# Performance work log

Hardware: AMD Instinct MI355X
Metric: run time of the kernel (lower is better)

## Reference

```python
import jax, jax.numpy as jnp
import numpy as np

EMBED = 768
HEADS = 12
HEAD_DIM = EMBED // HEADS
HIDDEN = int(EMBED * 4.0)
B, N = 2, 2048


def setup_inputs() -> dict:
    key = jax.random.key(0)
    ks = jax.random.split(key, 8)
    s = 0.02
    return {
        "x": jax.random.normal(ks[0], (B, N, EMBED), dtype=jnp.float32),
        "ln1_g": jnp.ones((EMBED,), jnp.float32),
        "ln1_b": jnp.zeros((EMBED,), jnp.float32),
        "qkv_w": jax.random.normal(ks[1], (3 * EMBED, EMBED), jnp.float32) * s,
        "qkv_b": jnp.zeros((3 * EMBED,), jnp.float32),
        "proj_w": jax.random.normal(ks[2], (EMBED, EMBED), jnp.float32) * s,
        "proj_b": jnp.zeros((EMBED,), jnp.float32),
        "ln2_g": jnp.ones((EMBED,), jnp.float32),
        "ln2_b": jnp.zeros((EMBED,), jnp.float32),
        "fc1_w": jax.random.normal(ks[3], (HIDDEN, EMBED), jnp.float32) * s,
        "fc1_b": jnp.zeros((HIDDEN,), jnp.float32),
        "fc2_w": jax.random.normal(ks[4], (EMBED, HIDDEN), jnp.float32) * s,
        "fc2_b": jnp.zeros((EMBED,), jnp.float32),
    }


def _layernorm(x, g, b, eps=1e-5):
    mu = jnp.mean(x, axis=-1, keepdims=True)
    var = jnp.var(x, axis=-1, keepdims=True)
    return (x - mu) * jax.lax.rsqrt(var + eps) * g + b


def reference(x, ln1_g, ln1_b, qkv_w, qkv_b, proj_w, proj_b,
              ln2_g, ln2_b, fc1_w, fc1_b, fc2_w, fc2_b):
    Bs, Ns, C = x.shape
    # --- attention (pre-norm) ---
    h = _layernorm(x, ln1_g, ln1_b)
    qkv = h @ qkv_w.T + qkv_b                      # [B,N,3C]
    qkv = qkv.reshape(Bs, Ns, 3, HEADS, HEAD_DIM)
    q, k, v = qkv[:, :, 0], qkv[:, :, 1], qkv[:, :, 2]   # [B,N,H,D]
    scale = HEAD_DIM ** -0.5
    attn = jnp.einsum('bqhd,bkhd->bhqk', q, k) * scale   # [B,H,N,N]
    attn = jax.nn.softmax(attn, axis=-1)
    o = jnp.einsum('bhqk,bkhd->bqhd', attn, v).reshape(Bs, Ns, C)
    x = x + (o @ proj_w.T + proj_b)
    # --- MLP (pre-norm) ---
    h = _layernorm(x, ln2_g, ln2_b)
    h = jax.nn.gelu(h @ fc1_w.T + fc1_b, approximate=False)  # torch GELU = erf
    x = x + (h @ fc2_w.T + fc2_b)
    return x
```

## Files before the change

### kernel.cpp

```cpp
#include <hip/hip_runtime.h>
#include <stdint.h>

#define EMBED  768
#define HEADS  12
#define HDIM   64
#define HIDDEN 3072
#define BSZ    2
#define SEQ    2048
#define NTOK   4096
#define QKVN   2304

typedef short short8 __attribute__((ext_vector_type(8)));
typedef float f32x4 __attribute__((ext_vector_type(4)));
typedef float float4v __attribute__((ext_vector_type(4)));
typedef unsigned short ushort4v __attribute__((ext_vector_type(4)));

__device__ __forceinline__ unsigned short f2bf(float f) {
    uint32_t x = __builtin_bit_cast(uint32_t, f);
    x = x + 0x7fffu + ((x >> 16) & 1u);
    return (unsigned short)(x >> 16);
}
__device__ __forceinline__ void load16(const void* g, void* l) {
    __builtin_amdgcn_global_load_lds((const __attribute__((address_space(1))) void*)g,
                                     (__attribute__((address_space(3))) void*)l, 16, 0, 0);
}

__global__ __launch_bounds__(256) void cvt4_k(const float* __restrict__ s0, unsigned short* __restrict__ o0, int n0,
                                              const float* __restrict__ s1, unsigned short* __restrict__ o1, int n1,
                                              const float* __restrict__ s2, unsigned short* __restrict__ o2, int n2,
                                              const float* __restrict__ s3, unsigned short* __restrict__ o3, int n3) {
    int i = blockIdx.x * blockDim.x + threadIdx.x;
    const int stride = gridDim.x * blockDim.x;
    const int tot = n0 + n1 + n2 + n3;
    for (; i < tot; i += stride) {
        const float* s; unsigned short* o; int j = i;
        if (j < n0) { s = s0; o = o0; }
        else if ((j -= n0) < n1) { s = s1; o = o1; }
        else if ((j -= n1) < n2) { s = s2; o = o2; }
        else { j -= n2; s = s3; o = o3; }
        float4v v = ((const float4v*)s)[j];
        ushort4v u;
#pragma unroll
        for (int t = 0; t < 4; t++) u[t] = f2bf(v[t]);
        ((ushort4v*)o)[j] = u;
    }
}

__global__ __launch_bounds__(256) void ln_k(const float* __restrict__ x,
                                            const float* __restrict__ g,
                                            const float* __restrict__ b,
                                            unsigned short* __restrict__ out) {
    const int row = blockIdx.x;
    const int t = threadIdx.x;
    const float* xr = x + (size_t)row * EMBED;
    float v0 = xr[t], v1 = xr[t + 256], v2 = xr[t + 512];
    float s = v0 + v1 + v2;
    float s2 = v0 * v0 + v1 * v1 + v2 * v2;
#pragma unroll
    for (int m = 1; m < 64; m <<= 1) { s += __shfl_xor(s, m); s2 += __shfl_xor(s2, m); }
    __shared__ float red[8];
    const int w = t >> 6;
    if ((t & 63) == 0) { red[w] = s; red[4 + w] = s2; }
    __syncthreads();
    s = red[0] + red[1] + red[2] + red[3];
    s2 = red[4] + red[5] + red[6] + red[7];
    const float mu = s * (1.0f / EMBED);
    const float var = s2 * (1.0f / EMBED) - mu * mu;
    const float rs = rsqrtf(var + 1e-5f);
    unsigned short* orow = out + (size_t)row * EMBED;
    orow[t]       = f2bf((v0 - mu) * rs * g[t]       + b[t]);
    orow[t + 256] = f2bf((v1 - mu) * rs * g[t + 256] + b[t + 256]);
    orow[t + 512] = f2bf((v2 - mu) * rs * g[t + 512] + b[t + 512]);
}

template <int EPI>
__global__ __launch_bounds__(256) void gemm_bt(const unsigned short* __restrict__ A,
                                               const unsigned short* __restrict__ W,
                                               const float* __restrict__ bias,
                                               const float* __restrict__ res,
                                               void* __restrict__ outp,
                                               unsigned short* __restrict__ vt,
                                               int M, int N, int K) {
    __shared__ __align__(16) char smem[36864];
    const int tid = threadIdx.x;
    const int w = tid >> 6, l = tid & 63;
    const int lr = l >> 4, lc = l & 15;
    const int nb = N >> 7;

    int bid = blockIdx.x;
    bid = (bid & 7) * (gridDim.x >> 3) + (bid >> 3);
    const int bx = bid % nb, by = bid / nb;
    const int row0 = by << 7, col0 = bx << 7;
    const int wr = w >> 1, wc = w & 1;
    const int srow = tid >> 2, skoff = (tid & 3) * 8;

    f32x4 acc[4][4] = {};

    const unsigned short* Ag0 = A + (size_t)(row0 + srow) * K + skoff;
    const unsigned short* Ag1 = A + (size_t)(row0 + 64 + srow) * K + skoff;
    const unsigned short* Wg0 = W + (size_t)(col0 + srow) * K + skoff;
    const unsigned short* Wg1 = W + (size_t)(col0 + 64 + srow) * K + skoff;

    auto Asb = [&](int buf) -> unsigned short* { return (unsigned short*)(smem + buf * 8192); };
    auto Bsb = [&](int buf) -> unsigned short* { return (unsigned short*)(smem + 16384 + buf * 8192); };

    auto stage = [&](int buf, int k0) {
        load16(Ag0 + k0, Asb(buf) + tid * 8);
        load16(Ag1 + k0, Asb(buf) + 2048 + tid * 8);
        load16(Wg0 + k0, Bsb(buf) + tid * 8);
        load16(Wg1 + k0, Bsb(buf) + 2048 + tid * 8);
    };
    auto compute = [&](int buf) {
        short8 af[4], bfr[4];
#pragma unroll
        for (int i = 0; i < 4; i++) af[i] = *(const short8*)&Asb(buf)[(wr * 64 + i * 16 + lc) * 32 + 8 * lr];
#pragma unroll
        for (int j = 0; j < 4; j++) bfr[j] = *(const short8*)&Bsb(buf)[(wc * 64 + j * 16 + lc) * 32 + 8 * lr];
#pragma unroll
        for (int i = 0; i < 4; i++)
#pragma unroll
            for (int j = 0; j < 4; j++)
                acc[i][j] = __builtin_amdgcn_mfma_f32_16x16x32_bf16(af[i], bfr[j], acc[i][j], 0, 0, 0);
    };

    stage(0, 0);
    for (int k0 = 0; k0 < K; k0 += 64) {
        __syncthreads();
        stage(1, k0 + 32);
        compute(0);
        __syncthreads();
        if (k0 + 64 < K) stage(0, k0 + 64);
        compute(1);
    }

    if (EPI == 0 || EPI == 2) {
        __syncthreads();
        unsigned short* ebuf = (unsigned short*)(smem + w * 9216);
        unsigned short* qo = (unsigned short*)outp;
#pragma unroll
        for (int i = 0; i < 4; i++)
#pragma unroll
            for (int j = 0; j < 4; j++) {
                const int col = col0 + wc * 64 + j * 16 + lc;
                const float bv = bias[col];
                float v[4];
#pragma unroll
                for (int r = 0; r < 4; r++) {
                    v[r] = acc[i][j][r] + bv;
                    if (EPI == 2) v[r] = 0.5f * v[r] * (1.0f + erff(v[r] * 0.70710678118f));
                }
                if (EPI == 0 && col >= 2 * EMBED) {
                    const int r0 = row0 + wr * 64 + i * 16 + 4 * lr;
                    const int hh = (col - 2 * EMBED) >> 6, d = col & 63;
                    const int bb = r0 >> 11, n0 = r0 & (SEQ - 1);
                    ushort4v pk;
#pragma unroll
                    for (int r = 0; r < 4; r++) pk[r] = f2bf(v[r]);
                    *(ushort4v*)&vt[((size_t)(bb * HEADS + hh) * HDIM + d) * SEQ + n0] = pk;
                }
#pragma unroll
                for (int r = 0; r < 4; r++)
                    ebuf[(i * 16 + 4 * lr + r) * 72 + j * 16 + lc] = f2bf(v[r]);
            }
        const int grow = row0 + wr * 64, gcol = col0 + wc * 64;
        const int rl0 = l >> 3, c8 = (l & 7) * 8;
#pragma unroll
        for (int k = 0; k < 8; k++) {
            const int rl = k * 8 + rl0;
            short8 vv = *(const short8*)&ebuf[rl * 72 + c8];
            *(short8*)&qo[(size_t)(grow + rl) * N + gcol + c8] = vv;
        }
    } else {
        float* fo = (float*)outp;
#pragma unroll
        for (int i = 0; i < 4; i++) {
            const int r0 = row0 + wr * 64 + i * 16 + 4 * lr;
#pragma unroll
            for (int j = 0; j < 4; j++) {
                const int col = col0 + wc * 64 + j * 16 + lc;
                const float bv = bias[col];
#pragma unroll
                for (int r = 0; r < 4; r++)
                    fo[(size_t)(r0 + r) * N + col] =
                        acc[i][j][r] + bv + res[(size_t)(r0 + r) * N + col];
            }
        }
    }
}

__global__ __launch_bounds__(256) void attn_k(const unsigned short* __restrict__ qkv,
                                              const unsigned short* __restrict__ vt,
                                              unsigned short* __restrict__ o_out) {
    __shared__ __align__(16) unsigned short Ks[128 * 64];
    __shared__ __align__(16) unsigned short Vs[64 * 128];
    __shared__ __align__(16) unsigned short Ps[4][16 * 136];

    const int tid = threadIdx.x;
    const int w = tid >> 6, l = tid & 63;
    const int lr = l >> 4, lc = l & 15;

    int f = blockIdx.x + blockIdx.y * gridDim.x;
    f = (f & 7) * ((gridDim.x * gridDim.y) >> 3) + (f >> 3);
    const int q0 = (f % gridDim.x) * 64;
    const int bh = f / gridDim.x;
    const int b = bh / HEADS, h = bh % HEADS;

    short8 aq[2];
#pragma unroll
    for (int kk = 0; kk < 2; kk++) {
        const int tok = b * SEQ + q0 + w * 16 + lc;
        aq[kk] = *(const short8*)&qkv[(size_t)tok * QKVN + h * HDIM + kk * 32 + 8 * lr];
    }

    f32x4 oacc[4] = {};
    float mst[4], lst[4];
#pragma unroll
    for (int r = 0; r < 4; r++) { mst[r] = -1e30f; lst[r] = 0.0f; }

    for (int kv0 = 0; kv0 < SEQ; kv0 += 128) {
        __syncthreads();
#pragma unroll
        for (int c = 0; c < 4; c++) {
            const int o = c * 4096 + tid * 16;
            const int krow = o >> 7, pc = o & 127;
            const int lcb = pc ^ ((krow & 7) << 4);
            load16(&qkv[(size_t)(b * SEQ + kv0 + krow) * QKVN + EMBED + h * HDIM + (lcb >> 1)],
                   (char*)Ks + o);
        }
#pragma unroll
        for (int c = 0; c < 4; c++) {
            const int o = c * 4096 + tid * 16;
            const int drow = o >> 8, pc = o & 255;
            const int lcb = pc ^ ((drow & 7) << 4);
            load16(&vt[(size_t)(bh * HDIM + drow) * SEQ + kv0 + (lcb >> 1)], (char*)Vs + o);
        }
        __syncthreads();

        f32x4 s[8] = {};
#pragma unroll
        for (int kk = 0; kk < 2; kk++) {
            short8 bk[8];
#pragma unroll
            for (int nj = 0; nj < 8; nj++) {
                const int krow = nj * 16 + lc;
                const int kb = kk * 64 + lr * 16;
                bk[nj] = *(const short8*)((const char*)Ks + krow * 128 + (kb ^ ((krow & 7) << 4)));
            }
#pragma unroll
            for (int nj = 0; nj < 8; nj++)
                s[nj] = __builtin_amdgcn_mfma_f32_16x16x32_bf16(aq[kk], bk[nj], s[nj], 0, 0, 0);
        }

#pragma unroll
        for (int r = 0; r < 4; r++) {
            float mt = s[0][r];
#pragma unroll
            for (int nj = 1; nj < 8; nj++) mt = fmaxf(mt, s[nj][r]);
#pragma unroll
            for (int m = 1; m < 16; m <<= 1) mt = fmaxf(mt, __shfl_xor(mt, m));
            const float mn = fmaxf(mst[r], mt);
            const float c_ = __expf((mst[r] - mn) * 0.125f);
            mst[r] = mn;
            float rsum = 0.0f;
#pragma unroll
            for (int nj = 0; nj < 8; nj++) {
                const float pv = __expf((s[nj][r] - mn) * 0.125f);
                s[nj][r] = pv;
                rsum += pv;
            }
#pragma unroll
            for (int m = 1; m < 16; m <<= 1) rsum += __shfl_xor(rsum, m);
            lst[r] = lst[r] * c_ + rsum;
#pragma unroll
            for (int dj = 0; dj < 4; dj++) oacc[dj][r] *= c_;
        }

#pragma unroll
        for (int nj = 0; nj < 8; nj++)
#pragma unroll
            for (int r = 0; r < 4; r++)
                Ps[w][(4 * lr + r) * 136 + nj * 16 + lc] = f2bf(s[nj][r]);

#pragma unroll
        for (int kk = 0; kk < 4; kk++) {
            short8 pa, bv[4];
            pa = *(const short8*)&Ps[w][lc * 136 + kk * 32 + 8 * lr];
#pragma unroll
            for (int dj = 0; dj < 4; dj++) {
                const int drow = dj * 16 + lc;
                const int kb = kk * 64 + lr * 16;
                bv[dj] = *(const short8*)((const char*)Vs + drow * 256 + (kb ^ ((drow & 7) << 4)));
            }
#pragma unroll
            for (int dj = 0; dj < 4; dj++)
                oacc[dj] = __builtin_amdgcn_mfma_f32_16x16x32_bf16(pa, bv[dj], oacc[dj], 0, 0, 0);
        }
    }

#pragma unroll
    for (int dj = 0; dj < 4; dj++)
#pragma unroll
        for (int r = 0; r < 4; r++) {
            const int q = q0 + w * 16 + 4 * lr + r;
            const int col = h * HDIM + dj * 16 + lc;
            o_out[(size_t)(b * SEQ + q) * EMBED + col] = f2bf(oacc[dj][r] / lst[r]);
        }
}

extern "C" void kernel_launch(void* const* d_in, const int* in_sizes, int n_in,
                              void* d_out, int out_size, void* d_ws, size_t ws_size,
                              hipStream_t stream) {
    const float* x      = (const float*)d_in[0];
    const float* ln1_g  = (const float*)d_in[1];
    const float* ln1_b  = (const float*)d_in[2];
    const float* qkv_w  = (const float*)d_in[3];
    const float* qkv_b  = (const float*)d_in[4];
    const float* proj_w = (const float*)d_in[5];
    const float* proj_b = (const float*)d_in[6];
    const float* ln2_g  = (const float*)d_in[7];
    const float* ln2_b  = (const float*)d_in[8];
    const float* fc1_w  = (const float*)d_in[9];
    const float* fc1_b  = (const float*)d_in[10];
    const float* fc2_w  = (const float*)d_in[11];
    const float* fc2_b  = (const float*)d_in[12];

    char* ws = (char*)d_ws;
    unsigned short* hbuf = (unsigned short*)(ws + 0);
    unsigned short* qkv  = (unsigned short*)(ws + 6291456);
    unsigned short* vt   = (unsigned short*)(ws + 25165824);
    float*          x2   = (float*)(ws + 31457280);
    unsigned short* gbuf = (unsigned short*)(ws + 6291456);
    unsigned short* wq   = (unsigned short*)(ws + 44040192);
    unsigned short* wp   = (unsigned short*)(ws + 47579136);
    unsigned short* w1   = (unsigned short*)(ws + 48758784);
    unsigned short* w2   = (unsigned short*)(ws + 53477376);

    cvt4_k<<<dim3(2048), 256, 0, stream>>>(qkv_w, wq, QKVN * EMBED / 4,
                                           proj_w, wp, EMBED * EMBED / 4,
                                           fc1_w, w1, HIDDEN * EMBED / 4,
                                           fc2_w, w2, EMBED * HIDDEN / 4);

    ln_k<<<dim3(NTOK), 256, 0, stream>>>(x, ln1_g, ln1_b, hbuf);

    gemm_bt<0><<<dim3((NTOK / 128) * (QKVN / 128)), 256, 0, stream>>>(
        hbuf, wq, qkv_b, nullptr, qkv, vt, NTOK, QKVN, EMBED);

    attn_k<<<dim3(SEQ / 64, BSZ * HEADS), 256, 0, stream>>>(qkv, vt, hbuf);

    gemm_bt<1><<<dim3((NTOK / 128) * (EMBED / 128)), 256, 0, stream>>>(
        hbuf, wp, proj_b, x, x2, nullptr, NTOK, EMBED, EMBED);

    ln_k<<<dim3(NTOK), 256, 0, stream>>>(x2, ln2_g, ln2_b, hbuf);

    gemm_bt<2><<<dim3((NTOK / 128) * (HIDDEN / 128)), 256, 0, stream>>>(
        hbuf, w1, fc1_b, nullptr, gbuf, nullptr, NTOK, HIDDEN, EMBED);

    gemm_bt<3><<<dim3((NTOK / 128) * (EMBED / 128)), 256, 0, stream>>>(
        gbuf, w2, fc2_b, x2, d_out, nullptr, NTOK, EMBED, HIDDEN);
}
```

Baseline: 310.4 us.

## Template GEMM tiles, triple-buffer K loop, and use exp2 softmax in attention

Makes the GEMM kernel a template over block and warp tile shapes. The QKV and FC1 GEMMs now use 256x256 tiles with 512 threads, and proj/FC2 keep 128x128. The K loop becomes a three-stage LDS pipeline with explicit vmcnt waits and one barrier per step instead of two, and the epilogue is staged in chunks of four row-tiles. In attention, the softmax uses exp2 with a scale folded into an FMA, and P is converted to bf16 by truncation instead of rounding. The larger tiles give more reuse but fewer blocks, more registers per thread, and lower occupancy. Truncating P adds a small bias in precision.

```diff
diff --git a/kernel.cpp b/kernel.cpp
--- a/kernel.cpp
+++ b/kernel.cpp
@@ -73,64 +73,78 @@
     orow[t + 512] = f2bf((v2 - mu) * rs * g[t + 512] + b[t + 512]);
 }
 
-template <int EPI>
-__global__ __launch_bounds__(256) void gemm_bt(const unsigned short* __restrict__ A,
-                                               const unsigned short* __restrict__ W,
-                                               const float* __restrict__ bias,
-                                               const float* __restrict__ res,
-                                               void* __restrict__ outp,
-                                               unsigned short* __restrict__ vt,
-                                               int M, int N, int K) {
-    __shared__ __align__(16) char smem[36864];
+template <int EPI, int BM, int BN, int WM, int WN>
+__global__ __launch_bounds__(WM * WN * 64, (WM * WN == 8) ? 2 : 3)
+void gemm_bt(const unsigned short* __restrict__ A,
+             const unsigned short* __restrict__ W,
+             const float* __restrict__ bias,
+             const float* __restrict__ res,
+             void* __restrict__ outp,
+             unsigned short* __restrict__ vt,
+             int M, int N, int K) {
+    constexpr int T = WM * WN * 64;
+    constexpr int MI = BM / (WM * 16);
+    constexpr int NJ = BN / (WN * 16);
+    constexpr int BUFB = (BM + BN) * 64;
+    constexpr int CH = T / 4;
+    __shared__ __align__(16) char smem[3 * BUFB];
+
     const int tid = threadIdx.x;
     const int w = tid >> 6, l = tid & 63;
     const int lr = l >> 4, lc = l & 15;
-    const int nb = N >> 7;
+    const int nb = N / BN;
 
     int bid = blockIdx.x;
     bid = (bid & 7) * (gridDim.x >> 3) + (bid >> 3);
     const int bx = bid % nb, by = bid / nb;
-    const int row0 = by << 7, col0 = bx << 7;
-    const int wr = w >> 1, wc = w & 1;
+    const int row0 = by * BM, col0 = bx * BN;
+    const int wr = w / WN, wc = w % WN;
     const int srow = tid >> 2, skoff = (tid & 3) * 8;
 
-    f32x4 acc[4][4] = {};
+    f32x4 acc[MI][NJ] = {};
 
     const unsigned short* Ag0 = A + (size_t)(row0 + srow) * K + skoff;
-    const unsigned short* Ag1 = A + (size_t)(row0 + 64 + srow) * K + skoff;
+    const unsigned short* Ag1 = A + (size_t)(row0 + CH + srow) * K + skoff;
     const unsigned short* Wg0 = W + (size_t)(col0 + srow) * K + skoff;
-    const unsigned short* Wg1 = W + (size_t)(col0 + 64 + srow) * K + skoff;
-
-    auto Asb = [&](int buf) -> unsigned short* { return (unsigned short*)(smem + buf * 8192); };
-    auto Bsb = [&](int buf) -> unsigned short* { return (unsigned short*)(smem + 16384 + buf * 8192); };
+    const unsigned short* Wg1 = W + (size_t)(col0 + CH + srow) * K + skoff;
 
     auto stage = [&](int buf, int k0) {
-        load16(Ag0 + k0, Asb(buf) + tid * 8);
-        load16(Ag1 + k0, Asb(buf) + 2048 + tid * 8);
-        load16(Wg0 + k0, Bsb(buf) + tid * 8);
-        load16(Wg1 + k0, Bsb(buf) + 2048 + tid * 8);
+        char* base = smem + buf * BUFB;
+        load16(Ag0 + k0, base + tid * 16);
+        load16(Ag1 + k0, base + T * 16 + tid * 16);
+        load16(Wg0 + k0, base + BM * 64 + tid * 16);
+        load16(Wg1 + k0, base + BM * 64 + T * 16 + tid * 16);
     };
     auto compute = [&](int buf) {
-        short8 af[4], bfr[4];
-#pragma unroll
-        for (int i = 0; i < 4; i++) af[i] = *(const short8*)&Asb(buf)[(wr * 64 + i * 16 + lc) * 32 + 8 * lr];
-#pragma unroll
-        for (int j = 0; j < 4; j++) bfr[j] = *(const short8*)&Bsb(buf)[(wc * 64 + j * 16 + lc) * 32 + 8 * lr];
-#pragma unroll
-        for (int i = 0; i < 4; i++)
-#pragma unroll
-            for (int j = 0; j < 4; j++)
-                acc[i][j] = __builtin_amdgcn_mfma_f32_16x16x32_bf16(af[i], bfr[j], acc[i][j], 0, 0, 0);
+        const unsigned short* Asb = (const unsigned short*)(smem + buf * BUFB);
+        const unsigned short* Bsb = (const unsigned short*)(smem + buf * BUFB + BM * 64);
+        short8 bfr[NJ];
+#pragma unroll
+        for (int j = 0; j < NJ; j++)
+            bfr[j] = *(const short8*)&Bsb[(wc * NJ * 16 + j * 16 + lc) * 32 + 8 * lr];
+#pragma unroll
+        for (int i = 0; i < MI; i++) {
+            short8 af = *(const short8*)&Asb[(wr * MI * 16 + i * 16 + lc) * 32 + 8 * lr];
+#pragma unroll
+            for (int j = 0; j < NJ; j++)
+                acc[i][j] = __builtin_amdgcn_mfma_f32_16x16x32_bf16(af, bfr[j], acc[i][j], 0, 0, 0);
+        }
     };
 
+    const int nt = K / 32;
     stage(0, 0);
-    for (int k0 = 0; k0 < K; k0 += 64) {
-        __syncthreads();
-        stage(1, k0 + 32);
-        compute(0);
-        __syncthreads();
-        if (k0 + 64 < K) stage(0, k0 + 64);
-        compute(1);
+    stage(1, 32);
+    int cur = 0;
+    for (int t = 0; t < nt; ++t) {
+        if (t + 1 < nt) asm volatile("s_waitcnt vmcnt(4)" ::: "memory");
+        else            asm volatile("s_waitcnt vmcnt(0)" ::: "memory");
+        __builtin_amdgcn_s_barrier();
+        if (t + 2 < nt) {
+            int nxt = cur + 2; if (nxt >= 3) nxt -= 3;
+            stage(nxt, (t + 2) * 32);
+        }
+        compute(cur);
+        cur = (cur == 2) ? 0 : cur + 1;
     }
 
     if (EPI == 0 || EPI == 2) {
@@ -138,46 +152,52 @@
         unsigned short* ebuf = (unsigned short*)(smem + w * 9216);
         unsigned short* qo = (unsigned short*)outp;
 #pragma unroll
-        for (int i = 0; i < 4; i++)
-#pragma unroll
-            for (int j = 0; j < 4; j++) {
-                const int col = col0 + wc * 64 + j * 16 + lc;
-                const float bv = bias[col];
-                float v[4];
-#pragma unroll
-                for (int r = 0; r < 4; r++) {
-                    v[r] = acc[i][j][r] + bv;
-                    if (EPI == 2) v[r] = 0.5f * v[r] * (1.0f + erff(v[r] * 0.70710678118f));
+        for (int ch = 0; ch < MI; ch += 4) {
+#pragma unroll
+            for (int i2 = 0; i2 < 4; i2++) {
+                const int i = ch + i2;
+#pragma unroll
+                for (int j = 0; j < NJ; j++) {
+                    const int col = col0 + wc * NJ * 16 + j * 16 + lc;
+                    const float bv = bias[col];
+                    float v[4];
+#pragma unroll
+                    for (int r = 0; r < 4; r++) {
+                        v[r] = acc[i][j][r] + bv;
+                        if (EPI == 2) v[r] = 0.5f * v[r] * (1.0f + erff(v[r] * 0.70710678118f));
+                    }
+                    if (EPI == 0 && col >= 2 * EMBED) {
+                        const int r0 = row0 + wr * MI * 16 + i * 16 + 4 * lr;
+                        const int hh = (col - 2 * EMBED) >> 6, d = col & 63;
+                        const int bb = r0 >> 11, n0 = r0 & (SEQ - 1);
+                        ushort4v pk;
+#pragma unroll
+                        for (int r = 0; r < 4; r++) pk[r] = f2bf(v[r]);
+                        *(ushort4v*)&vt[((size_t)(bb * HEADS + hh) * HDIM + d) * SEQ + n0] = pk;
+                    }
+#pragma unroll
+                    for (int r = 0; r < 4; r++)
+                        ebuf[(i2 * 16 + 4 * lr + r) * 72 + j * 16 + lc] = f2bf(v[r]);
                 }
-                if (EPI == 0 && col >= 2 * EMBED) {
-                    const int r0 = row0 + wr * 64 + i * 16 + 4 * lr;
-                    const int hh = (col - 2 * EMBED) >> 6, d = col & 63;
-                    const int bb = r0 >> 11, n0 = r0 & (SEQ - 1);
-                    ushort4v pk;
-#pragma unroll
-                    for (int r = 0; r < 4; r++) pk[r] = f2bf(v[r]);
-                    *(ushort4v*)&vt[((size_t)(bb * HEADS + hh) * HDIM + d) * SEQ + n0] = pk;
-                }
-#pragma unroll
-                for (int r = 0; r < 4; r++)
-                    ebuf[(i * 16 + 4 * lr + r) * 72 + j * 16 + lc] = f2bf(v[r]);
-            }
-        const int grow = row0 + wr * 64, gcol = col0 + wc * 64;
-        const int rl0 = l >> 3, c8 = (l & 7) * 8;
-#pragma unroll
-        for (int k = 0; k < 8; k++) {
-            const int rl = k * 8 + rl0;
-            short8 vv = *(const short8*)&ebuf[rl * 72 + c8];
-            *(short8*)&qo[(size_t)(grow + rl) * N + gcol + c8] = vv;
+            }
+            const int growc = row0 + wr * MI * 16 + ch * 16;
+            const int gcol = col0 + wc * NJ * 16;
+            const int rl0 = l >> 3, c8 = (l & 7) * 8;
+#pragma unroll
+            for (int k = 0; k < 8; k++) {
+                const int rl = k * 8 + rl0;
+                short8 vv = *(const short8*)&ebuf[rl * 72 + c8];
+                *(short8*)&qo[(size_t)(growc + rl) * N + gcol + c8] = vv;
+            }
         }
     } else {
         float* fo = (float*)outp;
 #pragma unroll
-        for (int i = 0; i < 4; i++) {
-            const int r0 = row0 + wr * 64 + i * 16 + 4 * lr;
-#pragma unroll
-            for (int j = 0; j < 4; j++) {
-                const int col = col0 + wc * 64 + j * 16 + lc;
+        for (int i = 0; i < MI; i++) {
+            const int r0 = row0 + wr * MI * 16 + i * 16 + 4 * lr;
+#pragma unroll
+            for (int j = 0; j < NJ; j++) {
+                const int col = col0 + wc * NJ * 16 + j * 16 + lc;
                 const float bv = bias[col];
 #pragma unroll
                 for (int r = 0; r < 4; r++)
@@ -212,10 +232,11 @@
         aq[kk] = *(const short8*)&qkv[(size_t)tok * QKVN + h * HDIM + kk * 32 + 8 * lr];
     }
 
+    const float C1 = 0.18033688011112042f;
     f32x4 oacc[4] = {};
-    float mst[4], lst[4];
-#pragma unroll
-    for (int r = 0; r < 4; r++) { mst[r] = -1e30f; lst[r] = 0.0f; }
+    float mstc[4], lst[4];
+#pragma unroll
+    for (int r = 0; r < 4; r++) { mstc[r] = -1e30f; lst[r] = 0.0f; }
 
     for (int kv0 = 0; kv0 < SEQ; kv0 += 128) {
         __syncthreads();
@@ -258,13 +279,13 @@
             for (int nj = 1; nj < 8; nj++) mt = fmaxf(mt, s[nj][r]);
 #pragma unroll
             for (int m = 1; m < 16; m <<= 1) mt = fmaxf(mt, __shfl_xor(mt, m));
-            const float mn = fmaxf(mst[r], mt);
-            const float c_ = __expf((mst[r] - mn) * 0.125f);
-            mst[r] = mn;
+            const float mnc = fmaxf(mstc[r], mt * C1);
+            const float c_ = exp2f(mstc[r] - mnc);
+            mstc[r] = mnc;
             float rsum = 0.0f;
 #pragma unroll
             for (int nj = 0; nj < 8; nj++) {
-                const float pv = __expf((s[nj][r] - mn) * 0.125f);
+                const float pv = exp2f(__builtin_fmaf(s[nj][r], C1, -mnc));
                 s[nj][r] = pv;
                 rsum += pv;
             }
@@ -279,7 +300,8 @@
         for (int nj = 0; nj < 8; nj++)
 #pragma unroll
             for (int r = 0; r < 4; r++)
-                Ps[w][(4 * lr + r) * 136 + nj * 16 + lc] = f2bf(s[nj][r]);
+                Ps[w][(4 * lr + r) * 136 + nj * 16 + lc] =
+                    (unsigned short)(__builtin_bit_cast(uint32_t, s[nj][r]) >> 16);
 
 #pragma unroll
         for (int kk = 0; kk < 4; kk++) {
@@ -342,19 +364,19 @@
 
     ln_k<<<dim3(NTOK), 256, 0, stream>>>(x, ln1_g, ln1_b, hbuf);
 
-    gemm_bt<0><<<dim3((NTOK / 128) * (QKVN / 128)), 256, 0, stream>>>(
+    gemm_bt<0, 256, 256, 2, 4><<<dim3((NTOK / 256) * (QKVN / 256)), 512, 0, stream>>>(
         hbuf, wq, qkv_b, nullptr, qkv, vt, NTOK, QKVN, EMBED);
 
     attn_k<<<dim3(SEQ / 64, BSZ * HEADS), 256, 0, stream>>>(qkv, vt, hbuf);
 
-    gemm_bt<1><<<dim3((NTOK / 128) * (EMBED / 128)), 256, 0, stream>>>(
+    gemm_bt<1, 128, 128, 2, 2><<<dim3((NTOK / 128) * (EMBED / 128)), 256, 0, stream>>>(
         hbuf, wp, proj_b, x, x2, nullptr, NTOK, EMBED, EMBED);
 
     ln_k<<<dim3(NTOK), 256, 0, stream>>>(x2, ln2_g, ln2_b, hbuf);
 
-    gemm_bt<2><<<dim3((NTOK / 128) * (HIDDEN / 128)), 256, 0, stream>>>(
+    gemm_bt<2, 256, 256, 2, 4><<<dim3((NTOK / 256) * (HIDDEN / 256)), 512, 0, stream>>>(
         hbuf, w1, fc1_b, nullptr, gbuf, nullptr, NTOK, HIDDEN, EMBED);
 
-    gemm_bt<3><<<dim3((NTOK / 128) * (EMBED / 128)), 256, 0, stream>>>(
+    gemm_bt<3, 128, 128, 2, 2><<<dim3((NTOK / 128) * (EMBED / 128)), 256, 0, stream>>>(
         gbuf, w2, fc2_b, x2, d_out, nullptr, NTOK, EMBED, HIDDEN);
 }
```

Measured after the change: 374.2 us. 1.21x slower.
